# Kernel tuning notes

Hardware: AMD Instinct MI355X
Metric: run time of the kernel (lower is better)

Reference implementation:

```python
import jax, jax.numpy as jnp
import numpy as np
from jax.scipy.special import logsumexp

N, D, M = 131072, 32, 256


def setup_inputs() -> dict:
    key = jax.random.key(0)
    k1, k2, k3 = jax.random.split(key, 3)
    X = jax.random.normal(k1, (N, D), dtype=jnp.float32)
    center = jax.random.uniform(k2, (M, D), dtype=jnp.float32)
    # cov_inv_sqrt near identity so det(cov_inv) ~ 1 (fit() would init it via Cholesky);
    # random-matrix init would make det overflow/underflow.
    cov_inv_sqrt = (jnp.eye(D, dtype=jnp.float32)[None, :, :]
                    + 0.02 * jax.random.normal(k3, (M, D, D), dtype=jnp.float32))
    weight = jnp.ones((M,), dtype=jnp.float32)
    threshold = jnp.zeros((1,), dtype=jnp.float32)
    return {"X": X, "center": center, "cov_inv_sqrt": cov_inv_sqrt,
            "weight": weight, "threshold": threshold}


def reference(X, center, cov_inv_sqrt, weight, threshold):
    # refresh(): equal_clusters=True branch
    w = jnp.abs(weight)
    pr = w / w.sum()                                            # [M]
    cov_inv = jnp.einsum('mij,mkj->mik', cov_inv_sqrt, cov_inv_sqrt)  # L L^T, [M,D,D]
    coef = pr * jnp.sqrt(jnp.linalg.det(cov_inv))               # [M]

    # Mahalanobis: q_ij = (x_i - c_j)^T A_j (x_i - c_j), expanded to avoid [N,M,D]:
    #   q_ij = xx_i . A_j_flat - 2 x_i . (A_j c_j) + c_j^T A_j c_j
    n, d = X.shape
    m = center.shape[0]
    A_flat = cov_inv.reshape(m, d * d)                          # [M, D*D]
    xx = (X[:, :, None] * X[:, None, :]).reshape(n, d * d)      # [N, D*D]
    term1 = xx @ A_flat.T                                       # [N, M]
    Ac = jnp.einsum('mkl,ml->mk', cov_inv, center)              # [M, D]
    term2 = X @ Ac.T                                            # [N, M]
    term3 = jnp.einsum('mk,mk->m', center, Ac)                  # [M]
    d_ij = -0.5 * (term1 - 2.0 * term2 + term3[None, :])        # [N, M]

    # weighted logsumexp over clusters: log sum_j coef_j exp(d_ij)
    ll = logsumexp(d_ij, axis=1, b=coef[None, :])               # [N]
    return ll - threshold[0]
```

## Files before the change

kernel.cpp:

```cpp
#include <hip/hip_runtime.h>
#include <hip/hip_bf16.h>
#include <math.h>

#define NPTS 131072
#define DIM 32
#define MCL 256
#define NSTEP 18
#define BPTS 128
#define THREADS 256

typedef __attribute__((ext_vector_type(8))) _Float16 f16x8;
typedef __attribute__((ext_vector_type(2))) _Float16 h2v;
typedef __attribute__((ext_vector_type(2))) unsigned u2v;
typedef __attribute__((ext_vector_type(4))) float f32x4;

__device__ __forceinline__ short f2h(float f) {
    _Float16 h = (_Float16)f;
    union { _Float16 h; short s; } X; X.h = h; return X.s;
}

__global__ __launch_bounds__(256) void gmm_prep(
    const float* __restrict__ center,
    const float* __restrict__ L,
    const float* __restrict__ weight,
    short* __restrict__ G,
    float* __restrict__ cst)
{
    const int m = blockIdx.x;
    const int t = threadIdx.x;
    __shared__ float Ls[DIM][DIM + 1];
    __shared__ float As[DIM][DIM + 1];
    __shared__ float Acs[DIM];
    __shared__ float red[DIM];

    const float* Lm = L + m * DIM * DIM;
    for (int k = t; k < DIM * DIM; k += 256)
        Ls[k >> 5][k & 31] = Lm[k];
    __syncthreads();

    for (int idx = t; idx < DIM * DIM; idx += 256) {
        const int j = idx >> 5, l = idx & 31;
        float a = 0.f;
        #pragma unroll
        for (int d = 0; d < DIM; ++d) a = fmaf(Ls[j][d], Ls[l][d], a);
        As[j][l] = a;
    }
    __syncthreads();

    if (t < DIM) {
        float a = 0.f;
        #pragma unroll
        for (int l = 0; l < DIM; ++l) a = fmaf(As[t][l], center[m * DIM + l], a);
        Acs[t] = a;
        red[t] = a * center[m * DIM + t];
    }
    __syncthreads();

    const int mt = m >> 4, ml = m & 15;
    for (int idx = t; idx < NSTEP * 32; idx += 256) {
        const int s = idx >> 5, k = idx & 31;
        float c;
        if (s == 0)       c = As[k][k] - 1.0f;
        else if (s <= 15) c = 2.0f * As[k][(k + s) & 31];
        else if (s == 16) c = (k < 16) ? 2.0f * As[k][k + 16] : -2.0f * Acs[k - 16];
        else              c = (k < 16) ? -2.0f * Acs[k + 16] : 0.0f;
        G[s * 8192 + mt * 512 + (k >> 3) * 128 + ml * 8 + (k & 7)] = f2h(c);
    }

    if (t < 64) {
        float logdet = 0.f;
        if (t < DIM) {
            float col[DIM];
            #pragma unroll
            for (int r2 = 0; r2 < DIM; ++r2) col[r2] = Ls[r2][t];
            float prodabs = 1.0f;
            #pragma unroll
            for (int k = 0; k < DIM; ++k) {
                const float pv  = __shfl(col[k], k, 64);
                const float rpv = 1.0f / pv;
                const float cjk = col[k];
                #pragma unroll
                for (int t2 = k + 1; t2 < DIM; ++t2) {
                    const float f = __shfl(col[t2], k, 64) * rpv;
                    col[t2] = fmaf(-f, cjk, col[t2]);
                }
                prodabs *= fabsf(pv);
            }
            logdet = logf(prodabs);
        }

        float wsp = 0.f;
        for (int j = t; j < MCL; j += 64) wsp += fabsf(weight[j]);
        #pragma unroll
        for (int d2 = 1; d2 < 64; d2 <<= 1) wsp += __shfl_xor(wsp, d2, 64);

        if (t == 0) {
            float t3 = 0.f;
            #pragma unroll
            for (int j = 0; j < DIM; ++j) t3 += red[j];
            cst[m] = logf(fabsf(weight[m])) - logf(wsp) + logdet - 0.5f * t3;
        }
    }
}

template<int J>
__device__ __forceinline__ unsigned wword(const u2v b0, const u2v b1, const u2v b2) {
    if constexpr (J < 2)      return b0[J];
    else if constexpr (J < 4) return b1[J - 2];
    else                      return b2[J - 4];
}

template<int OFF2, int Q>
__device__ __forceinline__ h2v wpair(const u2v b0, const u2v b1, const u2v b2) {
    static_assert((OFF2 & 1) == 0, "odd offsets eliminated by XhO copy");
    constexpr int wj = (OFF2 + 2 * Q) >> 1;
    union { unsigned u; h2v h; } X; X.u = wword<wj>(b0, b1, b2); return X.h;
}

template<int S, int Q, int OFF2>
__device__ __forceinline__ h2v mkpair(const h2v (&xp)[4], int kg,
                                      const u2v b0, const u2v b1, const u2v b2) {
    if constexpr (S == 0) {
        return xp[Q] * xp[Q];
    } else {
        const h2v wp = wpair<OFF2, Q>(b0, b1, b2);
        if constexpr (S == 16) {
            return (kg < 2) ? (h2v)(xp[Q] * wp) : wp;
        } else if constexpr (S == 17) {
            const h2v z = { (_Float16)0.f, (_Float16)0.f };
            return (kg < 2) ? wp : z;
        } else {
            return xp[Q] * wp;
        }
    }
}

template<int S>
__device__ __forceinline__ void k_step(
    const short* __restrict__ gw,
    const short* __restrict__ Xh,
    const short* __restrict__ XhO,
    const int (&rowh)[4],
    const h2v (&xp)[4][4],
    f16x8 (&bf)[8],
    f32x4 (&acc)[4][8],
    int kg)
{
    constexpr int shv  = (S == 17) ? 16 : S;
    constexpr bool odd = (shv & 1) != 0;
    constexpr int sh2  = odd ? (shv - 1) : shv;
    constexpr int off2 = sh2 & 3;
    const int bq = ((kg * 8 + sh2) & 31) & ~3;

    f16x8 af[4];
    #pragma unroll
    for (int i = 0; i < 4; ++i) {
        u2v b0 = {}, b1 = {}, b2 = {};
        if constexpr (S != 0) {
            const short* xr = (odd ? XhO : Xh) + rowh[i] + bq;
            b0 = *(const u2v*)(xr);
            b1 = *(const u2v*)(xr + 4);
            if constexpr (off2 != 0) b2 = *(const u2v*)(xr + 8);
        }
        union { f16x8 v; h2v p[4]; } U;
        U.p[0] = mkpair<S, 0, off2>(xp[i], kg, b0, b1, b2);
        U.p[1] = mkpair<S, 1, off2>(xp[i], kg, b0, b1, b2);
        U.p[2] = mkpair<S, 2, off2>(xp[i], kg, b0, b1, b2);
        U.p[3] = mkpair<S, 3, off2>(xp[i], kg, b0, b1, b2);
        af[i] = U.v;
    }

    #pragma unroll
    for (int j = 0; j < 8; ++j) {
        #pragma unroll
        for (int i = 0; i < 4; ++i)
            acc[i][j] = __builtin_amdgcn_mfma_f32_16x16x32_f16(
                af[i], bf[j], acc[i][j], 0, 0, 0);
        if constexpr (S + 1 < NSTEP)
            bf[j] = *(const f16x8*)(gw + (size_t)(S + 1) * 8192 + j * 512);
    }
    __builtin_amdgcn_sched_barrier(0);
}

template<int S>
__device__ __forceinline__ void k_loop(
    const short* __restrict__ gw, const short* __restrict__ Xh,
    const short* __restrict__ XhO,
    const int (&rowh)[4], const h2v (&xp)[4][4],
    f16x8 (&bf)[8], f32x4 (&acc)[4][8], int kg)
{
    k_step<S>(gw, Xh, XhO, rowh, xp, bf, acc, kg);
    if constexpr (S + 1 < NSTEP)
        k_loop<S + 1>(gw, Xh, XhO, rowh, xp, bf, acc, kg);
}

__global__ __launch_bounds__(THREADS, 2) void gmm_mfma(
    const float* __restrict__ X,
    const short* __restrict__ G,
    const float* __restrict__ cstw,
    const float* __restrict__ thr,
    float* __restrict__ out)
{
    __shared__ __attribute__((aligned(16))) short Xh[BPTS * 44];
    __shared__ __attribute__((aligned(16))) short XhO[BPTS * 44];
    __shared__ float nrm_s[BPTS];
    __shared__ float cst_s[MCL];
    __shared__ float lse_m[BPTS];
    __shared__ float lse_d[BPTS];

    const int tid  = threadIdx.x;
    const int lane = tid & 63;
    const int w    = tid >> 6;
    const int wr   = w & 1;
    const int wc   = w >> 1;
    const int r    = lane & 15;
    const int kg   = lane >> 4;
    const int P0   = blockIdx.x * BPTS;

    const short* gw = G + wc * 4096 + lane * 8;

    int rowh[4];
    h2v xp[4][4];
    #pragma unroll
    for (int i = 0; i < 4; ++i) {
        const int row = wr * 64 + i * 16 + r;
        rowh[i] = row * 44;
        const float4* xg = reinterpret_cast<const float4*>(
            X + (size_t)(P0 + row) * DIM + kg * 8);
        const float4 a = xg[0], b = xg[1];
        xp[i][0] = h2v{ (_Float16)a.x, (_Float16)a.y };
        xp[i][1] = h2v{ (_Float16)a.z, (_Float16)a.w };
        xp[i][2] = h2v{ (_Float16)b.x, (_Float16)b.y };
        xp[i][3] = h2v{ (_Float16)b.z, (_Float16)b.w };
    }

    {
        const int p = tid >> 1, hf = tid & 1;
        const float4* Xg = reinterpret_cast<const float4*>(
            X + (size_t)(P0 + p) * DIM + hf * 16);
        float part = 0.f;
        #pragma unroll
        for (int q = 0; q < 4; ++q) {
            const float4 v = Xg[q];
            const int kb = hf * 16 + 4 * q;
            const short h0 = f2h(v.x), h1 = f2h(v.y), h2 = f2h(v.z), h3 = f2h(v.w);
            Xh[p * 44 + kb + 0] = h0;
            Xh[p * 44 + kb + 1] = h1;
            Xh[p * 44 + kb + 2] = h2;
            Xh[p * 44 + kb + 3] = h3;
            if (!hf && q < 2) {
                Xh[p * 44 + 32 + kb + 0] = h0;
                Xh[p * 44 + 32 + kb + 1] = h1;
                Xh[p * 44 + 32 + kb + 2] = h2;
                Xh[p * 44 + 32 + kb + 3] = h3;
            }
            const int i0 = (kb - 1) & 31;
            XhO[p * 44 + i0] = h0;
            XhO[p * 44 + kb + 0] = h1;
            XhO[p * 44 + kb + 1] = h2;
            XhO[p * 44 + kb + 2] = h3;
            if (i0 < 8)       XhO[p * 44 + 32 + i0] = h0;
            if (kb + 0 < 8) { XhO[p * 44 + 32 + kb + 0] = h1; }
            if (kb + 1 < 8) { XhO[p * 44 + 32 + kb + 1] = h2; }
            if (kb + 2 < 8) { XhO[p * 44 + 32 + kb + 2] = h3; }
            part = fmaf(v.x, v.x, part); part = fmaf(v.y, v.y, part);
            part = fmaf(v.z, v.z, part); part = fmaf(v.w, v.w, part);
        }
        part += __shfl_xor(part, 1, 64);
        if (!hf) nrm_s[p] = part;
        cst_s[tid] = cstw[tid];
    }

    f16x8 bf[8];
    #pragma unroll
    for (int j = 0; j < 8; ++j)
        bf[j] = *(const f16x8*)(gw + j * 512);

    __syncthreads();

    f32x4 acc[4][8] = {};
    k_loop<0>(gw, Xh, XhO, rowh, xp, bf, acc, kg);

    float cstr[8];
    #pragma unroll
    for (int j = 0; j < 8; ++j)
        cstr[j] = cst_s[wc * 128 + j * 16 + r];

    float mx[16], sm[16];
    #pragma unroll
    for (int i = 0; i < 4; ++i)
        #pragma unroll
        for (int rg = 0; rg < 4; ++rg) {
            const int sl = i * 4 + rg;
            float m_ = -1e30f;
            #pragma unroll
            for (int j = 0; j < 8; ++j)
                m_ = fmaxf(m_, fmaf(acc[i][j][rg], -0.5f, cstr[j]));
            #pragma unroll
            for (int d = 1; d < 16; d <<= 1)
                m_ = fmaxf(m_, __shfl_xor(m_, d, 64));
            float s_ = 0.f;
            #pragma unroll
            for (int j = 0; j < 8; ++j)
                s_ += __expf(fmaf(acc[i][j][rg], -0.5f, cstr[j]) - m_);
            #pragma unroll
            for (int d = 1; d < 16; d <<= 1)
                s_ += __shfl_xor(s_, d, 64);
            mx[sl] = m_; sm[sl] = s_;
        }

    if (wc == 0 && r == 0) {
        #pragma unroll
        for (int i = 0; i < 4; ++i)
            #pragma unroll
            for (int rg = 0; rg < 4; ++rg) {
                const int p2 = wr * 64 + i * 16 + kg * 4 + rg;
                lse_m[p2] = mx[i * 4 + rg];
                lse_d[p2] = sm[i * 4 + rg];
            }
    }
    __syncthreads();
    if (wc == 1 && r == 0) {
        const float thrv = thr[0];
        #pragma unroll
        for (int i = 0; i < 4; ++i)
            #pragma unroll
            for (int rg = 0; rg < 4; ++rg) {
                const int sl = i * 4 + rg;
                const int p2 = wr * 64 + i * 16 + kg * 4 + rg;
                const float om = lse_m[p2], os = lse_d[p2];
                const float nm = fmaxf(mx[sl], om);
                const float ss = sm[sl] * __expf(mx[sl] - nm) + os * __expf(om - nm);
                out[P0 + p2] = nm + __logf(ss) - 0.5f * nrm_s[p2] - thrv;
            }
    }
}

extern "C" void kernel_launch(void* const* d_in, const int* in_sizes, int n_in,
                              void* d_out, int out_size, void* d_ws, size_t ws_size,
                              hipStream_t stream)
{
    const float* X      = (const float*)d_in[0];
    const float* center = (const float*)d_in[1];
    const float* L      = (const float*)d_in[2];
    const float* weight = (const float*)d_in[3];
    const float* thr    = (const float*)d_in[4];
    float* out = (float*)d_out;

    float* cst = (float*)d_ws;
    short* G   = (short*)((char*)d_ws + 1024);

    gmm_prep<<<MCL, 256, 0, stream>>>(center, L, weight, G, cst);
    gmm_mfma<<<NPTS / BPTS, THREADS, 0, stream>>>(X, G, cst, thr, out);
}
```

Baseline: 64.03 us.

## Split cluster columns into two chunks with online logsumexp merge, raise occupancy

Each wave now processes its 128 clusters in two passes of 64, keeping a 4x4 accumulator tile instead of 4x8. Partial max and sum from the first pass go to shared memory and are merged online with the second pass. The smaller register footprint lets launch bounds ask for 3 blocks per SIMD instead of 2. In exchange, the A-fragment construction and X loads from LDS run twice, and an extra shared-memory round trip plus extra exp work is added.

```diff
diff --git a/kernel.cpp b/kernel.cpp
--- a/kernel.cpp
+++ b/kernel.cpp
@@ -135,15 +135,15 @@
     }
 }
 
-template<int S>
+template<int S, int CH>
 __device__ __forceinline__ void k_step(
     const short* __restrict__ gw,
     const short* __restrict__ Xh,
     const short* __restrict__ XhO,
     const int (&rowh)[4],
     const h2v (&xp)[4][4],
-    f16x8 (&bf)[8],
-    f32x4 (&acc)[4][8],
+    f16x8 (&bf)[4],
+    f32x4 (&acc)[4][4],
     int kg)
 {
     constexpr int shv  = (S == 17) ? 16 : S;
@@ -171,30 +171,32 @@
     }
 
     #pragma unroll
-    for (int j = 0; j < 8; ++j) {
+    for (int j = 0; j < 4; ++j) {
         #pragma unroll
         for (int i = 0; i < 4; ++i)
             acc[i][j] = __builtin_amdgcn_mfma_f32_16x16x32_f16(
                 af[i], bf[j], acc[i][j], 0, 0, 0);
         if constexpr (S + 1 < NSTEP)
-            bf[j] = *(const f16x8*)(gw + (size_t)(S + 1) * 8192 + j * 512);
+            bf[j] = *(const f16x8*)(gw + (size_t)(S + 1) * 8192 + CH * 2048 + j * 512);
+        else if constexpr (CH == 0)
+            bf[j] = *(const f16x8*)(gw + 2048 + j * 512);
     }
     __builtin_amdgcn_sched_barrier(0);
 }
 
-template<int S>
+template<int S, int CH>
 __device__ __forceinline__ void k_loop(
     const short* __restrict__ gw, const short* __restrict__ Xh,
     const short* __restrict__ XhO,
     const int (&rowh)[4], const h2v (&xp)[4][4],
-    f16x8 (&bf)[8], f32x4 (&acc)[4][8], int kg)
+    f16x8 (&bf)[4], f32x4 (&acc)[4][4], int kg)
 {
-    k_step<S>(gw, Xh, XhO, rowh, xp, bf, acc, kg);
+    k_step<S, CH>(gw, Xh, XhO, rowh, xp, bf, acc, kg);
     if constexpr (S + 1 < NSTEP)
-        k_loop<S + 1>(gw, Xh, XhO, rowh, xp, bf, acc, kg);
-}
-
-__global__ __launch_bounds__(THREADS, 2) void gmm_mfma(
+        k_loop<S + 1, CH>(gw, Xh, XhO, rowh, xp, bf, acc, kg);
+}
+
+__global__ __launch_bounds__(THREADS, 3) void gmm_mfma(
     const float* __restrict__ X,
     const short* __restrict__ G,
     const float* __restrict__ cstw,
@@ -205,6 +207,8 @@
     __shared__ __attribute__((aligned(16))) short XhO[BPTS * 44];
     __shared__ float nrm_s[BPTS];
     __shared__ float cst_s[MCL];
+    __shared__ float ch_m[4][64];
+    __shared__ float ch_d[4][64];
     __shared__ float lse_m[BPTS];
     __shared__ float lse_d[BPTS];
 
@@ -271,43 +275,85 @@
         cst_s[tid] = cstw[tid];
     }
 
-    f16x8 bf[8];
+    f16x8 bf[4];
     #pragma unroll
-    for (int j = 0; j < 8; ++j)
+    for (int j = 0; j < 4; ++j)
         bf[j] = *(const f16x8*)(gw + j * 512);
 
     __syncthreads();
 
-    f32x4 acc[4][8] = {};
-    k_loop<0>(gw, Xh, XhO, rowh, xp, bf, acc, kg);
-
-    float cstr[8];
-    #pragma unroll
-    for (int j = 0; j < 8; ++j)
-        cstr[j] = cst_s[wc * 128 + j * 16 + r];
+    f32x4 acc[4][4] = {};
+
+    k_loop<0, 0>(gw, Xh, XhO, rowh, xp, bf, acc, kg);
+    {
+        float cstr[4];
+        #pragma unroll
+        for (int j = 0; j < 4; ++j)
+            cstr[j] = cst_s[wc * 128 + j * 16 + r];
+        #pragma unroll
+        for (int i = 0; i < 4; ++i)
+            #pragma unroll
+            for (int rg = 0; rg < 4; ++rg) {
+                float m_ = -1e30f;
+                #pragma unroll
+                for (int j = 0; j < 4; ++j)
+                    m_ = fmaxf(m_, fmaf(acc[i][j][rg], -0.5f, cstr[j]));
+                #pragma unroll
+                for (int d = 1; d < 16; d <<= 1)
+                    m_ = fmaxf(m_, __shfl_xor(m_, d, 64));
+                float s_ = 0.f;
+                #pragma unroll
+                for (int j = 0; j < 4; ++j)
+                    s_ += __expf(fmaf(acc[i][j][rg], -0.5f, cstr[j]) - m_);
+                #pragma unroll
+                for (int d = 1; d < 16; d <<= 1)
+                    s_ += __shfl_xor(s_, d, 64);
+                if (r == 0) {
+                    ch_m[w][i * 16 + kg * 4 + rg] = m_;
+                    ch_d[w][i * 16 + kg * 4 + rg] = s_;
+                }
+            }
+        #pragma unroll
+        for (int i = 0; i < 4; ++i)
+            #pragma unroll
+            for (int j = 0; j < 4; ++j)
+                acc[i][j] = f32x4{0.f, 0.f, 0.f, 0.f};
+    }
+
+    k_loop<0, 1>(gw, Xh, XhO, rowh, xp, bf, acc, kg);
 
     float mx[16], sm[16];
-    #pragma unroll
-    for (int i = 0; i < 4; ++i)
-        #pragma unroll
-        for (int rg = 0; rg < 4; ++rg) {
-            const int sl = i * 4 + rg;
-            float m_ = -1e30f;
-            #pragma unroll
-            for (int j = 0; j < 8; ++j)
-                m_ = fmaxf(m_, fmaf(acc[i][j][rg], -0.5f, cstr[j]));
-            #pragma unroll
-            for (int d = 1; d < 16; d <<= 1)
-                m_ = fmaxf(m_, __shfl_xor(m_, d, 64));
-            float s_ = 0.f;
-            #pragma unroll
-            for (int j = 0; j < 8; ++j)
-                s_ += __expf(fmaf(acc[i][j][rg], -0.5f, cstr[j]) - m_);
-            #pragma unroll
-            for (int d = 1; d < 16; d <<= 1)
-                s_ += __shfl_xor(s_, d, 64);
-            mx[sl] = m_; sm[sl] = s_;
-        }
+    {
+        float cstr[4];
+        #pragma unroll
+        for (int j = 0; j < 4; ++j)
+            cstr[j] = cst_s[wc * 128 + 64 + j * 16 + r];
+        #pragma unroll
+        for (int i = 0; i < 4; ++i)
+            #pragma unroll
+            for (int rg = 0; rg < 4; ++rg) {
+                const int sl = i * 4 + rg;
+                float m_ = -1e30f;
+                #pragma unroll
+                for (int j = 0; j < 4; ++j)
+                    m_ = fmaxf(m_, fmaf(acc[i][j][rg], -0.5f, cstr[j]));
+                #pragma unroll
+                for (int d = 1; d < 16; d <<= 1)
+                    m_ = fmaxf(m_, __shfl_xor(m_, d, 64));
+                float s_ = 0.f;
+                #pragma unroll
+                for (int j = 0; j < 4; ++j)
+                    s_ += __expf(fmaf(acc[i][j][rg], -0.5f, cstr[j]) - m_);
+                #pragma unroll
+                for (int d = 1; d < 16; d <<= 1)
+                    s_ += __shfl_xor(s_, d, 64);
+                const float m0 = ch_m[w][i * 16 + kg * 4 + rg];
+                const float s0 = ch_d[w][i * 16 + kg * 4 + rg];
+                const float nm = fmaxf(m_, m0);
+                sm[sl] = s_ * __expf(m_ - nm) + s0 * __expf(m0 - nm);
+                mx[sl] = nm;
+            }
+    }
 
     if (wc == 0 && r == 0) {
         #pragma unroll
```

New measurement: 75.72 us. +18.3%, slower.
